# Kernel tuning notes

Hardware: AMD Instinct MI355X
Metric: run time of the kernel (lower is better)

## Reference

```python
import jax, jax.numpy as jnp
import numpy as np
import math

N_PATCH = 32768
DIM = 512
L_TOK = 64
W_SIZE = 64
STRIDE = 32


def setup_inputs() -> dict:
    key = jax.random.key(0)
    ks = jax.random.split(key, 12)
    d = DIM
    inp = {
        'feats': jax.random.normal(ks[0], (N_PATCH, d), dtype=jnp.float32),
        'coords': jax.random.uniform(ks[1], (N_PATCH, 2), dtype=jnp.float32),
        'mask': jnp.zeros((N_PATCH,), dtype=bool),
        'z': jax.random.normal(ks[2], (L_TOK, d), dtype=jnp.float32),
        'Wq': jax.random.normal(ks[3], (d, d), dtype=jnp.float32) / math.sqrt(d),
        'Wk': jax.random.normal(ks[4], (d, d), dtype=jnp.float32) / math.sqrt(d),
        'Wv': jax.random.normal(ks[5], (d, d), dtype=jnp.float32) / math.sqrt(d),
        'w1': jax.random.normal(ks[6], (d, 2), dtype=jnp.float32) / math.sqrt(2.0),
        'b1': jnp.zeros((d,), dtype=jnp.float32),
        'w2': jax.random.normal(ks[7], (d, d), dtype=jnp.float32) / math.sqrt(d),
        'b2': jnp.zeros((d,), dtype=jnp.float32),
        'Wo': jax.random.normal(ks[8], (d, d), dtype=jnp.float32) / math.sqrt(d),
        'bo': jnp.zeros((d,), dtype=jnp.float32),
    }
    return inp


def _lstcwa(feats, coords, z, Wq, Wk, Wv, w1, b1, w2, b2, Wo, bo):
    # mask is all-False -> feats kept as-is; N divisible by L -> equal segments
    N, D = feats.shape
    L = z.shape[0]
    n = N // L                       # patches per segment
    nwin = -(-n // STRIDE)           # windows per segment (ceil)

    # window offsets within a segment, [nwin, w]; last window truncated via mask
    off = jnp.arange(nwin)[:, None] * STRIDE + jnp.arange(W_SIZE)[None, :]
    valid = off < n                  # [nwin, w]
    idx = jnp.arange(L)[:, None, None] * n + jnp.minimum(off, n - 1)[None]  # [L,nwin,w]

    q = z @ Wq.T                     # [L, D]
    kf = feats @ Wk.T                # [N, D]
    vf = feats @ Wv.T

    k_win = kf[idx]                  # [L, nwin, w, D]
    v_win = vf[idx]
    c_win = coords[idx]              # [L, nwin, w, 2]

    vf32 = valid.astype(feats.dtype)                      # [nwin, w]
    cnt = vf32.sum(-1)                                    # [nwin]
    c_mean = jnp.einsum('lnwc,nw->lnc', c_win, vf32) / cnt[None, :, None]
    delta = (c_win - c_mean[:, :, None, :]) * vf32[None, :, :, None]

    pos = jax.nn.relu(delta @ w1.T + b1) @ w2.T + b2      # [L, nwin, w, D]
    k_win = k_win + pos

    logits = jnp.einsum('ld,lnwd->lnw', q, k_win) / math.sqrt(D)
    logits = jnp.where(valid[None], logits, -1e9)
    attn = jax.nn.softmax(logits, axis=-1)                # [L, nwin, w]

    z_win = jnp.einsum('lnw,lnwd->lnd', attn, v_win)      # [L, nwin, D]
    # return_alpha=False path: z_l_acc / max(1, len(attn_acc)=0) -> SUM over windows
    Z = z_win.sum(1)                                      # [L, D]
    return Z @ Wo.T + bo


def reference(feats, coords, mask, z, Wq, Wk, Wv, w1, b1, w2, b2, Wo, bo):
    # mask is all-False by construction (static shapes under jit)
    return _lstcwa(feats, coords, z, Wq, Wk, Wv, w1, b1, w2, b2, Wo, bo)
```

## Files before the change

### kernel.cpp

```cpp
#include <hip/hip_runtime.h>
#include <math.h>

#define DIMV 512
#define LTOK 64
#define SEG  512
#define NWIN 16
#define WSZ  64
#define INV_SQRT_D 0.044194173824159216f

__device__ __forceinline__ float wave_sum(float v) {
#pragma unroll
  for (int m = 1; m < 64; m <<= 1) v += __shfl_xor(v, m, 64);
  return v;
}
__device__ __forceinline__ float wave_max(float v) {
#pragma unroll
  for (int m = 1; m < 64; m <<= 1) v = fmaxf(v, __shfl_xor(v, m, 64));
  return v;
}

__global__ __launch_bounds__(256, 4) void k_q(const float* __restrict__ z,
    const float* __restrict__ Wq, const float* __restrict__ coords,
    float* __restrict__ q, float* __restrict__ cmean)
{
  int l = blockIdx.x >> 4, c = blockIdx.x & 15;
  int wave = threadIdx.x >> 6, lane = threadIdx.x & 63;
  int e0 = lane << 3;
  const float* zp = z + l * DIMV + e0;
  float x0[8];
  *(float4*)&x0[0] = *(const float4*)zp;
  *(float4*)&x0[4] = *(const float4*)(zp + 4);
  int d0 = c * 32 + wave * 8;
  float rf[8][8];
#pragma unroll
  for (int k = 0; k < 8; ++k) {
    const float* rp = Wq + (size_t)(d0 + k) * DIMV + e0;
    *(float4*)&rf[k][0] = *(const float4*)rp;
    *(float4*)&rf[k][4] = *(const float4*)(rp + 4);
  }
#pragma unroll
  for (int k = 0; k < 8; ++k) {
    float p = 0.f;
#pragma unroll
    for (int j = 0; j < 8; ++j) p = fmaf(rf[k][j], x0[j], p);
    p = wave_sum(p);
    if (lane == k) q[l * DIMV + d0 + k] = p;
  }
  if (wave == 0) {
    int n = c;
    int nvalid = (n == 15) ? 32 : 64;
    bool v = lane < nvalid;
    float cx = 0.f, cy = 0.f;
    if (v) {
      const float* cp = coords + ((size_t)(l * SEG + n * 32 + lane)) * 2;
      cx = cp[0]; cy = cp[1];
    }
    float inv = 1.0f / (float)nvalid;
    float mx = wave_sum(cx) * inv;
    float my = wave_sum(cy) * inv;
    if (lane == 0) {
      cmean[(l * NWIN + n) * 2]     = mx;
      cmean[(l * NWIN + n) * 2 + 1] = my;
    }
  }
}

__global__ __launch_bounds__(256) void k_qproj(const float* __restrict__ q,
    const float* __restrict__ Wk, const float* __restrict__ w2,
    const float* __restrict__ b2, float* __restrict__ qk,
    float* __restrict__ qw2, float* __restrict__ qb2)
{
  int l = blockIdx.x >> 3, ec = blockIdx.x & 7;
  int wave = threadIdx.x >> 6, lane = threadIdx.x & 63;
  int t = threadIdx.x;
  __shared__ float qs[DIMV];
  __shared__ float pk[4][64], pw[4][64];
  qs[t] = q[l * DIMV + t];
  qs[t + 256] = q[l * DIMV + t + 256];
  __syncthreads();
  int e = ec * 64 + lane;
  int d0 = wave * 128;
  float ak = 0.f, aw = 0.f;
#pragma unroll 8
  for (int dd = 0; dd < 128; ++dd) {
    int d = d0 + dd;
    float qd = qs[d];
    ak = fmaf(qd, Wk[(size_t)d * DIMV + e], ak);
    aw = fmaf(qd, w2[(size_t)d * DIMV + e], aw);
  }
  pk[wave][lane] = ak;
  pw[wave][lane] = aw;
  __syncthreads();
  if (wave == 0) {
    qk[l * DIMV + e] = pk[0][lane] + pk[1][lane] + pk[2][lane] + pk[3][lane];
  } else if (wave == 1) {
    qw2[l * DIMV + e] = pw[0][lane] + pw[1][lane] + pw[2][lane] + pw[3][lane];
  } else if (wave == 2 && ec == 0) {
    int e0 = lane << 3;
    float pb = 0.f;
#pragma unroll
    for (int j = 0; j < 8; ++j) pb = fmaf(qs[e0 + j], b2[e0 + j], pb);
    pb = wave_sum(pb);
    if (lane == 0) qb2[l] = pb;
  }
}

__global__ __launch_bounds__(256, 8) void k_dot(
    const float* __restrict__ feats, const float* __restrict__ qk,
    float* __restrict__ dts)
{
  int l = blockIdx.x >> 5, c = blockIdx.x & 31;
  int wave = threadIdx.x >> 6, lane = threadIdx.x & 63;
  int e0 = lane << 3;
  int rbase = c * 16 + wave * 4;
  const float* fbase = feats + ((size_t)(l * SEG + rbase)) * DIMV;
  float rf[4][8];
#pragma unroll
  for (int k = 0; k < 4; ++k) {
    const float* rp = fbase + (size_t)k * DIMV + e0;
    *(float4*)&rf[k][0] = *(const float4*)rp;
    *(float4*)&rf[k][4] = *(const float4*)(rp + 4);
  }
  float qk8[8];
  {
    const float* p = qk + l * DIMV + e0;
    *(float4*)&qk8[0] = *(const float4*)p;
    *(float4*)&qk8[4] = *(const float4*)(p + 4);
  }
#pragma unroll
  for (int k = 0; k < 4; ++k) {
    float s = 0.f;
#pragma unroll
    for (int j = 0; j < 8; ++j) s = fmaf(qk8[j], rf[k][j], s);
    s = wave_sum(s);
    if (lane == k) dts[l * SEG + rbase + k] = s;
  }
}

__global__ __launch_bounds__(256, 4) void k_soft(
    const float* __restrict__ coords, const float* __restrict__ cmean,
    const float* __restrict__ dts,   const float* __restrict__ qw2,
    const float* __restrict__ qb2,   const float* __restrict__ w1,
    const float* __restrict__ b1,    float* __restrict__ attn)
{
  int widx = blockIdx.x;
  int l = widx >> 4, n = widx & 15;
  int t = threadIdx.x;
  int p = t & 63, qd = t >> 6;
  __shared__ float w1s[2 * DIMV], b1s[DIMV], qws[DIMV], part[4][WSZ];
#pragma unroll
  for (int i = 0; i < 4; ++i) w1s[t + 256 * i] = w1[t + 256 * i];
#pragma unroll
  for (int i = 0; i < 2; ++i) {
    b1s[t + 256 * i] = b1[t + 256 * i];
    qws[t + 256 * i] = qw2[l * DIMV + t + 256 * i];
  }
  __syncthreads();
  int nvalid = (n == 15) ? 32 : 64;
  int off = n * 32 + p;
  int row = (p < nvalid) ? off : (SEG - 1);
  float dx = coords[((size_t)(l * SEG + row)) * 2]     - cmean[(l * NWIN + n) * 2];
  float dy = coords[((size_t)(l * SEG + row)) * 2 + 1] - cmean[(l * NWIN + n) * 2 + 1];
  float acc = 0.f;
  int d0 = qd * 128;
#pragma unroll 4
  for (int dd = 0; dd < 128; ++dd) {
    int d = d0 + dd;
    float h = fmaf(dx, w1s[2 * d], fmaf(dy, w1s[2 * d + 1], b1s[d]));
    acc = fmaf(fmaxf(h, 0.f), qws[d], acc);
  }
  part[qd][p] = acc;
  __syncthreads();
  if (t < 64) {
    float pos = part[0][p] + part[1][p] + part[2][p] + part[3][p];
    float lg = (p < nvalid) ? (dts[l * SEG + off] + pos + qb2[l]) * INV_SQRT_D
                            : -1e9f;
    float m = wave_max(lg);
    float ex = __expf(lg - m);
    float s = wave_sum(ex);
    attn[(size_t)widx * WSZ + p] = ex / s;
  }
}

__global__ __launch_bounds__(256, 8) void k_wsum(
    const float* __restrict__ feats, const float* __restrict__ attn,
    float* __restrict__ upart)
{
  int l = blockIdx.x >> 4, c = blockIdx.x & 15;
  int wave = threadIdx.x >> 6, lane = threadIdx.x & 63;
  int e0 = lane << 3, t = threadIdx.x;
  __shared__ float gs[32];
  __shared__ float upacc[4][DIMV];
  if (t < 32) {
    float g = attn[((size_t)(l * NWIN) + c) * WSZ + t];
    if (c > 0) g += attn[((size_t)(l * NWIN) + c - 1) * WSZ + 32 + t];
    gs[t] = g;
  }
  __syncthreads();
  int rbase = wave * 8;
  const float* fbase = feats + ((size_t)(l * SEG + c * 32 + rbase)) * DIMV;
  float u8[8];
#pragma unroll
  for (int j = 0; j < 8; ++j) u8[j] = 0.f;
#pragma unroll
  for (int k = 0; k < 8; ++k) {
    float g = gs[rbase + k];
    const float* rp = fbase + (size_t)k * DIMV + e0;
    float f8[8];
    *(float4*)&f8[0] = *(const float4*)rp;
    *(float4*)&f8[4] = *(const float4*)(rp + 4);
#pragma unroll
    for (int j = 0; j < 8; ++j) u8[j] = fmaf(g, f8[j], u8[j]);
  }
  *(float4*)&upacc[wave][e0]     = *(float4*)&u8[0];
  *(float4*)&upacc[wave][e0 + 4] = *(float4*)&u8[4];
  __syncthreads();
#pragma unroll
  for (int i = 0; i < 2; ++i) {
    int e = t + 256 * i;
    upart[((size_t)(l * NWIN) + c) * DIMV + e] =
        upacc[0][e] + upacc[1][e] + upacc[2][e] + upacc[3][e];
  }
}

__global__ __launch_bounds__(256, 4) void k_uv(const float* __restrict__ upart,
    const float* __restrict__ Wv, float* __restrict__ tbuf)
{
  int l = blockIdx.x >> 4, c = blockIdx.x & 15;
  int wave = threadIdx.x >> 6, lane = threadIdx.x & 63;
  int e0 = lane << 3;
  float u8[8];
#pragma unroll
  for (int j = 0; j < 8; ++j) u8[j] = 0.f;
#pragma unroll
  for (int cc = 0; cc < NWIN; ++cc) {
    const float* up = upart + ((size_t)(l * NWIN) + cc) * DIMV + e0;
    float4 a = *(const float4*)up;
    float4 b = *(const float4*)(up + 4);
    u8[0] += a.x; u8[1] += a.y; u8[2] += a.z; u8[3] += a.w;
    u8[4] += b.x; u8[5] += b.y; u8[6] += b.z; u8[7] += b.w;
  }
  int f0 = c * 32 + wave * 8;
  float rf[8][8];
#pragma unroll
  for (int k = 0; k < 8; ++k) {
    const float* rp = Wv + (size_t)(f0 + k) * DIMV + e0;
    *(float4*)&rf[k][0] = *(const float4*)rp;
    *(float4*)&rf[k][4] = *(const float4*)(rp + 4);
  }
#pragma unroll
  for (int k = 0; k < 8; ++k) {
    float p = 0.f;
#pragma unroll
    for (int j = 0; j < 8; ++j) p = fmaf(rf[k][j], u8[j], p);
    p = wave_sum(p);
    if (lane == k) tbuf[l * DIMV + f0 + k] = p;
  }
}

__global__ __launch_bounds__(256, 4) void k_out(const float* __restrict__ tbuf,
    const float* __restrict__ Wo, const float* __restrict__ bo,
    float* __restrict__ out)
{
  int l = blockIdx.x >> 4, c = blockIdx.x & 15;
  int wave = threadIdx.x >> 6, lane = threadIdx.x & 63;
  int e0 = lane << 3;
  const float* tp = tbuf + l * DIMV + e0;
  float x0[8];
  *(float4*)&x0[0] = *(const float4*)tp;
  *(float4*)&x0[4] = *(const float4*)(tp + 4);
  int d0 = c * 32 + wave * 8;
  float rf[8][8];
#pragma unroll
  for (int k = 0; k < 8; ++k) {
    const float* rp = Wo + (size_t)(d0 + k) * DIMV + e0;
    *(float4*)&rf[k][0] = *(const float4*)rp;
    *(float4*)&rf[k][4] = *(const float4*)(rp + 4);
  }
#pragma unroll
  for (int k = 0; k < 8; ++k) {
    float p = 0.f;
#pragma unroll
    for (int j = 0; j < 8; ++j) p = fmaf(rf[k][j], x0[j], p);
    p = wave_sum(p);
    if (lane == k) out[l * DIMV + d0 + k] = p + bo[d0 + k];
  }
}

extern "C" void kernel_launch(void* const* d_in, const int* in_sizes, int n_in,
                              void* d_out, int out_size, void* d_ws, size_t ws_size,
                              hipStream_t stream) {
  (void)in_sizes; (void)n_in; (void)out_size; (void)ws_size;
  const float* feats  = (const float*)d_in[0];
  const float* coords = (const float*)d_in[1];
  const float* z   = (const float*)d_in[3];
  const float* Wq  = (const float*)d_in[4];
  const float* Wk  = (const float*)d_in[5];
  const float* Wv  = (const float*)d_in[6];
  const float* w1  = (const float*)d_in[7];
  const float* b1  = (const float*)d_in[8];
  const float* w2  = (const float*)d_in[9];
  const float* b2  = (const float*)d_in[10];
  const float* Wo  = (const float*)d_in[11];
  const float* bo  = (const float*)d_in[12];
  float* out = (float*)d_out;

  float* q     = (float*)d_ws;
  float* qk    = q     + LTOK * DIMV;
  float* qw2   = qk    + LTOK * DIMV;
  float* qb2   = qw2   + LTOK * DIMV;
  float* cmean = qb2   + LTOK;
  float* dts   = cmean + LTOK * NWIN * 2;
  float* attn  = dts   + LTOK * SEG;
  float* tbuf  = attn  + LTOK * NWIN * WSZ;
  float* upart = tbuf  + LTOK * DIMV;

  hipLaunchKernelGGL(k_q,     dim3(LTOK * NWIN),  dim3(256), 0, stream,
                     z, Wq, coords, q, cmean);
  hipLaunchKernelGGL(k_qproj, dim3(LTOK * 8),     dim3(256), 0, stream,
                     q, Wk, w2, b2, qk, qw2, qb2);
  hipLaunchKernelGGL(k_dot,   dim3(LTOK * 32),    dim3(256), 0, stream,
                     feats, qk, dts);
  hipLaunchKernelGGL(k_soft,  dim3(LTOK * NWIN),  dim3(256), 0, stream,
                     coords, cmean, dts, qw2, qb2, w1, b1, attn);
  hipLaunchKernelGGL(k_wsum,  dim3(LTOK * NWIN),  dim3(256), 0, stream,
                     feats, attn, upart);
  hipLaunchKernelGGL(k_uv,    dim3(LTOK * NWIN),  dim3(256), 0, stream,
                     upart, Wv, tbuf);
  hipLaunchKernelGGL(k_out,   dim3(LTOK * NWIN),  dim3(256), 0, stream,
                     tbuf, Wo, bo, out);
}
```

Measured before the change: 68.66 us.

## Fuse key dot, softmax and weighted sum into one per-window attention kernel

```diff
diff --git a/kernel.cpp b/kernel.cpp
--- a/kernel.cpp
+++ b/kernel.cpp
@@ -105,43 +105,11 @@
   }
 }
 
-__global__ __launch_bounds__(256, 8) void k_dot(
-    const float* __restrict__ feats, const float* __restrict__ qk,
-    float* __restrict__ dts)
-{
-  int l = blockIdx.x >> 5, c = blockIdx.x & 31;
-  int wave = threadIdx.x >> 6, lane = threadIdx.x & 63;
-  int e0 = lane << 3;
-  int rbase = c * 16 + wave * 4;
-  const float* fbase = feats + ((size_t)(l * SEG + rbase)) * DIMV;
-  float rf[4][8];
-#pragma unroll
-  for (int k = 0; k < 4; ++k) {
-    const float* rp = fbase + (size_t)k * DIMV + e0;
-    *(float4*)&rf[k][0] = *(const float4*)rp;
-    *(float4*)&rf[k][4] = *(const float4*)(rp + 4);
-  }
-  float qk8[8];
-  {
-    const float* p = qk + l * DIMV + e0;
-    *(float4*)&qk8[0] = *(const float4*)p;
-    *(float4*)&qk8[4] = *(const float4*)(p + 4);
-  }
-#pragma unroll
-  for (int k = 0; k < 4; ++k) {
-    float s = 0.f;
-#pragma unroll
-    for (int j = 0; j < 8; ++j) s = fmaf(qk8[j], rf[k][j], s);
-    s = wave_sum(s);
-    if (lane == k) dts[l * SEG + rbase + k] = s;
-  }
-}
-
-__global__ __launch_bounds__(256, 4) void k_soft(
+__global__ __launch_bounds__(256, 4) void k_pos(
     const float* __restrict__ coords, const float* __restrict__ cmean,
-    const float* __restrict__ dts,   const float* __restrict__ qw2,
-    const float* __restrict__ qb2,   const float* __restrict__ w1,
-    const float* __restrict__ b1,    float* __restrict__ attn)
+    const float* __restrict__ qw2,   const float* __restrict__ qb2,
+    const float* __restrict__ w1,    const float* __restrict__ b1,
+    float* __restrict__ pos)
 {
   int widx = blockIdx.x;
   int l = widx >> 4, n = widx & 15;
@@ -172,55 +140,84 @@
   part[qd][p] = acc;
   __syncthreads();
   if (t < 64) {
-    float pos = part[0][p] + part[1][p] + part[2][p] + part[3][p];
-    float lg = (p < nvalid) ? (dts[l * SEG + off] + pos + qb2[l]) * INV_SQRT_D
-                            : -1e9f;
-    float m = wave_max(lg);
-    float ex = __expf(lg - m);
-    float s = wave_sum(ex);
-    attn[(size_t)widx * WSZ + p] = ex / s;
-  }
-}
-
-__global__ __launch_bounds__(256, 8) void k_wsum(
-    const float* __restrict__ feats, const float* __restrict__ attn,
-    float* __restrict__ upart)
-{
-  int l = blockIdx.x >> 4, c = blockIdx.x & 15;
+    pos[(size_t)widx * WSZ + p] =
+        part[0][p] + part[1][p] + part[2][p] + part[3][p] + qb2[l];
+  }
+}
+
+__global__ __launch_bounds__(512, 1) void k_attn(
+    const float* __restrict__ feats, const float* __restrict__ qk,
+    const float* __restrict__ pos,  float* __restrict__ upart)
+{
+  int bid = blockIdx.x;
+  int swz = (bid & 7) * 128 + (bid >> 3);
+  int l = swz >> 4, n = swz & 15;
   int wave = threadIdx.x >> 6, lane = threadIdx.x & 63;
   int e0 = lane << 3, t = threadIdx.x;
-  __shared__ float gs[32];
-  __shared__ float upacc[4][DIMV];
-  if (t < 32) {
-    float g = attn[((size_t)(l * NWIN) + c) * WSZ + t];
-    if (c > 0) g += attn[((size_t)(l * NWIN) + c - 1) * WSZ + 32 + t];
-    gs[t] = g;
-  }
-  __syncthreads();
-  int rbase = wave * 8;
-  const float* fbase = feats + ((size_t)(l * SEG + c * 32 + rbase)) * DIMV;
+  int base = n * 32;
+  int nvalid = (n == 15) ? 32 : 64;
+
+  __shared__ float tile[WSZ][DIMV];
+  __shared__ float lg[WSZ];
+  __shared__ float upacc[8][DIMV];
+
+  float qk8[8];
+  {
+    const float* p = qk + l * DIMV + e0;
+    *(float4*)&qk8[0] = *(const float4*)p;
+    *(float4*)&qk8[4] = *(const float4*)(p + 4);
+  }
+  const float* fwin = feats + ((size_t)(l * SEG + base)) * DIMV;
+
+#pragma unroll
+  for (int k = 0; k < 8; ++k) {
+    int r = wave * 8 + k;
+    float f8[8];
+    if (r < nvalid) {
+      const float* rp = fwin + (size_t)r * DIMV + e0;
+      *(float4*)&f8[0] = *(const float4*)rp;
+      *(float4*)&f8[4] = *(const float4*)(rp + 4);
+    } else {
+#pragma unroll
+      for (int j = 0; j < 8; ++j) f8[j] = 0.f;
+    }
+    *(float4*)&tile[r][e0]     = *(float4*)&f8[0];
+    *(float4*)&tile[r][e0 + 4] = *(float4*)&f8[4];
+    float p = 0.f;
+#pragma unroll
+    for (int j = 0; j < 8; ++j) p = fmaf(qk8[j], f8[j], p);
+    p = wave_sum(p);
+    if (lane == k) lg[r] = p;
+  }
+  __syncthreads();
+
+  float posv = pos[((size_t)(l * NWIN) + n) * WSZ + lane];
+  float plg = (lane < nvalid) ? (lg[lane] + posv) * INV_SQRT_D : -1e9f;
+  float m = wave_max(plg);
+  float ex = __expf(plg - m);
+  float s = wave_sum(ex);
+  float my_attn = ex / s;
+
   float u8[8];
 #pragma unroll
   for (int j = 0; j < 8; ++j) u8[j] = 0.f;
 #pragma unroll
   for (int k = 0; k < 8; ++k) {
-    float g = gs[rbase + k];
-    const float* rp = fbase + (size_t)k * DIMV + e0;
+    int r = wave * 8 + k;
+    float a = __shfl(my_attn, r, 64);
     float f8[8];
-    *(float4*)&f8[0] = *(const float4*)rp;
-    *(float4*)&f8[4] = *(const float4*)(rp + 4);
-#pragma unroll
-    for (int j = 0; j < 8; ++j) u8[j] = fmaf(g, f8[j], u8[j]);
+    *(float4*)&f8[0] = *(float4*)&tile[r][e0];
+    *(float4*)&f8[4] = *(float4*)&tile[r][e0 + 4];
+#pragma unroll
+    for (int j = 0; j < 8; ++j) u8[j] = fmaf(a, f8[j], u8[j]);
   }
   *(float4*)&upacc[wave][e0]     = *(float4*)&u8[0];
   *(float4*)&upacc[wave][e0 + 4] = *(float4*)&u8[4];
   __syncthreads();
-#pragma unroll
-  for (int i = 0; i < 2; ++i) {
-    int e = t + 256 * i;
-    upart[((size_t)(l * NWIN) + c) * DIMV + e] =
-        upacc[0][e] + upacc[1][e] + upacc[2][e] + upacc[3][e];
-  }
+  float acc = 0.f;
+#pragma unroll
+  for (int wv = 0; wv < 8; ++wv) acc += upacc[wv][t];
+  upart[((size_t)(l * NWIN) + n) * DIMV + t] = acc;
 }
 
 __global__ __launch_bounds__(256, 4) void k_uv(const float* __restrict__ upart,
@@ -310,23 +307,20 @@
   float* qw2   = qk    + LTOK * DIMV;
   float* qb2   = qw2   + LTOK * DIMV;
   float* cmean = qb2   + LTOK;
-  float* dts   = cmean + LTOK * NWIN * 2;
-  float* attn  = dts   + LTOK * SEG;
-  float* tbuf  = attn  + LTOK * NWIN * WSZ;
+  float* pos   = cmean + LTOK * NWIN * 2;
+  float* tbuf  = pos   + LTOK * NWIN * WSZ;
   float* upart = tbuf  + LTOK * DIMV;
 
-  hipLaunchKernelGGL(k_q,     dim3(LTOK * NWIN),  dim3(256), 0, stream,
+  hipLaunchKernelGGL(k_q,     dim3(LTOK * NWIN), dim3(256), 0, stream,
                      z, Wq, coords, q, cmean);
-  hipLaunchKernelGGL(k_qproj, dim3(LTOK * 8),     dim3(256), 0, stream,
+  hipLaunchKernelGGL(k_qproj, dim3(LTOK * 8),    dim3(256), 0, stream,
                      q, Wk, w2, b2, qk, qw2, qb2);
-  hipLaunchKernelGGL(k_dot,   dim3(LTOK * 32),    dim3(256), 0, stream,
-                     feats, qk, dts);
-  hipLaunchKernelGGL(k_soft,  dim3(LTOK * NWIN),  dim3(256), 0, stream,
-                     coords, cmean, dts, qw2, qb2, w1, b1, attn);
-  hipLaunchKernelGGL(k_wsum,  dim3(LTOK * NWIN),  dim3(256), 0, stream,
-                     feats, attn, upart);
-  hipLaunchKernelGGL(k_uv,    dim3(LTOK * NWIN),  dim3(256), 0, stream,
+  hipLaunchKernelGGL(k_pos,   dim3(LTOK * NWIN), dim3(256), 0, stream,
+                     coords, cmean, qw2, qb2, w1, b1, pos);
+  hipLaunchKernelGGL(k_attn,  dim3(LTOK * NWIN), dim3(512), 0, stream,
+                     feats, qk, pos, upart);
+  hipLaunchKernelGGL(k_uv,    dim3(LTOK * NWIN), dim3(256), 0, stream,
                      upart, Wv, tbuf);
-  hipLaunchKernelGGL(k_out,   dim3(LTOK * NWIN),  dim3(256), 0, stream,
+  hipLaunchKernelGGL(k_out,   dim3(LTOK * NWIN), dim3(256), 0, stream,
                      tbuf, Wo, bo, out);
 }
```

New measurement: 71.28 us. 1.04x slower.
